# Kernel tuning notes

Hardware: AMD Instinct MI355X
Metric: run time of the kernel (lower is better)

The kernel has to match this reference:

```python
import jax, jax.numpy as jnp
import numpy as np


def _ln(x):
    m = jnp.mean(x, axis=-1, keepdims=True)
    v = jnp.var(x, axis=-1, keepdims=True)
    return (x - m) * jax.lax.rsqrt(v + 1e-5)


def _forward(ql, cl, plm, ada_g_w, ada_g_b, ada_b_w, wq, bq, wk, wv, z_ln_g, z_ln_b, wz, wg, wo, sg_w, sg_b, ada2_g_w, ada2_g_b, ada2_b_w, ff1, ff2, ff3, sg2_w, sg2_b, n_queries, n_keys):
    B, N, C = ql.shape
    NB, _, D = wq.shape
    H = wz.shape[-1]
    DH = D // H
    # AF3-style 32x128 blocked local attention bias (additive mask), as in source
    centers = jnp.arange(N // n_queries + 1, dtype=jnp.float32) * n_queries + (n_queries / 2 - 0.5)
    pos = jnp.arange(N, dtype=jnp.float32)
    row = jnp.abs(pos[:, None] - centers[None, :]) < n_queries / 2   # [N, n_centers]
    col = jnp.abs(pos[:, None] - centers[None, :]) < n_keys / 2     # [N, n_centers]
    BIG = jnp.float32(1e10)
    blm = jnp.sum((row[:, None, :] & col[None, :, :]).astype(jnp.float32), axis=-1) * BIG - BIG  # [N, N], 0 or -1e10
    s_ln = _ln(cl)  # conditioning signal, shared LN across blocks
    a = ql
    for i in range(NB):  # DiffusionTransformer (AF3 Alg 23)
        # AttentionPairBias with AdaLN conditioning (Alg 24/26)
        x = jax.nn.sigmoid(s_ln @ ada_g_w[i] + ada_g_b[i]) * _ln(a) + s_ln @ ada_b_w[i]
        q = (x @ wq[i] + bq[i]).reshape(B, N, H, DH)
        k = (x @ wk[i]).reshape(B, N, H, DH)
        v = (x @ wv[i]).reshape(B, N, H, DH)
        zb = jnp.einsum('bqkc,ch->bhqk', _ln(plm) * z_ln_g[i] + z_ln_b[i], wz[i])  # pair bias
        logits = jnp.einsum('bqhd,bkhd->bhqk', q, k) * (1.0 / np.sqrt(DH)) + zb + blm[None, None]
        p = jax.nn.softmax(logits, axis=-1)
        o = jnp.einsum('bhqk,bkhd->bqhd', p, v)
        g = jax.nn.sigmoid(x @ wg[i]).reshape(B, N, H, DH)
        attn = (g * o).reshape(B, N, D) @ wo[i]
        b_out = jax.nn.sigmoid(s_ln @ sg_w[i] + sg_b[i]) * attn  # adaLN-zero style output gate
        # ConditionedTransitionBlock (Alg 25, SwiGLU)
        y = jax.nn.sigmoid(s_ln @ ada2_g_w[i] + ada2_g_b[i]) * _ln(a) + s_ln @ ada2_b_w[i]
        ff = jax.nn.silu(y @ ff1[i]) * (y @ ff2[i])
        t = jax.nn.sigmoid(s_ln @ sg2_w[i] + sg2_b[i]) * (ff @ ff3[i])
        a = b_out + t
    return a


def setup_inputs() -> dict:
    key = jax.random.key(0)
    B, N, C, CZ = 1, 3072, 128, 16
    H, DH, NB, CT = 4, 32, 3, 256  # CT = n_transition * C
    D = H * DH
    ks = jax.random.split(key, 32)
    it = iter(range(32))
    def r(shape, s=0.02):
        return jax.random.normal(ks[next(it)], shape, dtype=jnp.float32) * s
    inp = {
        'ql': jax.random.normal(ks[next(it)], (B, N, C), jnp.float32),
        'cl': jax.random.normal(ks[next(it)], (B, N, C), jnp.float32),
        'plm': jax.random.normal(ks[next(it)], (B, N, N, CZ), jnp.float32),
        'ada_g_w': r((NB, C, C)), 'ada_g_b': jnp.zeros((NB, C), jnp.float32), 'ada_b_w': r((NB, C, C)),
        'wq': r((NB, C, D)), 'bq': jnp.zeros((NB, D), jnp.float32), 'wk': r((NB, C, D)), 'wv': r((NB, C, D)),
        'z_ln_g': jnp.ones((NB, CZ), jnp.float32), 'z_ln_b': jnp.zeros((NB, CZ), jnp.float32), 'wz': r((NB, CZ, H)),
        'wg': r((NB, C, D)), 'wo': r((NB, D, C)),
        'sg_w': r((NB, C, C)), 'sg_b': jnp.full((NB, C), -2.0, jnp.float32),
        'ada2_g_w': r((NB, C, C)), 'ada2_g_b': jnp.zeros((NB, C), jnp.float32), 'ada2_b_w': r((NB, C, C)),
        'ff1': r((NB, C, CT)), 'ff2': r((NB, C, CT)), 'ff3': r((NB, CT, C)),
        'sg2_w': r((NB, C, C)), 'sg2_b': jnp.full((NB, C), -2.0, jnp.float32),
        'n_queries': 32, 'n_keys': 128,
    }
    return inp


def reference(ql, cl, plm, ada_g_w, ada_g_b, ada_b_w, wq, bq, wk, wv, z_ln_g, z_ln_b, wz, wg, wo, sg_w, sg_b, ada2_g_w, ada2_g_b, ada2_b_w, ff1, ff2, ff3, sg2_w, sg2_b, n_queries, n_keys):
    return _forward(ql, cl, plm, ada_g_w, ada_g_b, ada_b_w, wq, bq, wk, wv, z_ln_g, z_ln_b, wz, wg, wo, sg_w, sg_b, ada2_g_w, ada2_g_b, ada2_b_w, ff1, ff2, ff3, sg2_w, sg2_b, n_queries, n_keys)
```

## Files before the change

### kernel.cpp

```cpp
#include <hip/hip_runtime.h>
#include <cmath>

#define NTOK 3072
#define NBLK 3
#define PSS 133

__device__ __forceinline__ float sig(float v) { return 1.0f / (1.0f + expf(-v)); }

struct Params {
    const float *ql, *cl, *plm;
    const float *ada_g_w, *ada_g_b, *ada_b_w;
    const float *wq, *bq, *wk, *wv;
    const float *z_ln_g, *z_ln_b, *wz;
    const float *wg, *wo, *sg_w, *sg_b;
    const float *ada2_g_w, *ada2_g_b, *ada2_b_w;
    const float *ff1, *ff2, *ff3, *sg2_w, *sg2_b;
    float *anew, *attn, *qkvg, *ffb, *zb, *G;
    float *out;
};

__device__ __forceinline__ float4 ln_row32(float4 v)
{
    float s = v.x + v.y + v.z + v.w;
#pragma unroll
    for (int m = 1; m < 32; m <<= 1) s += __shfl_xor(s, m);
    float mean = s * (1.0f / 128.0f);
    float d0 = v.x - mean, d1 = v.y - mean, d2 = v.z - mean, d3 = v.w - mean;
    float var = d0 * d0 + d1 * d1 + d2 * d2 + d3 * d3;
#pragma unroll
    for (int m = 1; m < 32; m <<= 1) var += __shfl_xor(var, m);
    float rs = 1.0f / sqrtf(var * (1.0f / 128.0f) + 1e-5f);
    return make_float4(d0 * rs, d1 * rs, d2 * rs, d3 * rs);
}

__global__ __launch_bounds__(256) void k0_cond(Params P)
{
    int tid = threadIdx.x, bid = blockIdx.x;
    const size_t NC = (size_t)NTOK * 128;
    if (bid < 1728) {
        __shared__ __align__(16) float smA[32 * 132];
        int x8 = bid & 7, rest = bid >> 3;
        int tl = rest % 12, unit = rest / 12;
        int kind = unit % 6, i = unit / 6;
        int row0 = (x8 * 12 + tl) * 32;
#pragma unroll
        for (int it = 0; it < 4; it++) {
            int fo = (tid + it * 256) * 4, r = fo >> 7, c = fo & 127;
            *(float4*)&smA[r * 132 + c] = *(const float4*)&P.cl[(size_t)(row0 + r) * 128 + c];
        }
        __syncthreads();
        int hw = tid >> 5, cq = (tid & 31) * 4;
#pragma unroll
        for (int rr = 0; rr < 4; rr++) {
            int r = hw * 4 + rr;
            float4 n = ln_row32(*(float4*)&smA[r * 132 + cq]);
            *(float4*)&smA[r * 132 + cq] = n;
        }
        __syncthreads();
        const float* W; const float* bias = nullptr; bool dosig = false;
        switch (kind) {
            case 0:  W = P.ada_g_w  + (size_t)i * 16384; bias = P.ada_g_b  + i * 128; dosig = true; break;
            case 1:  W = P.ada_b_w  + (size_t)i * 16384; break;
            case 2:  W = P.ada2_g_w + (size_t)i * 16384; bias = P.ada2_g_b + i * 128; dosig = true; break;
            case 3:  W = P.ada2_b_w + (size_t)i * 16384; break;
            case 4:  W = P.sg_w     + (size_t)i * 16384; bias = P.sg_b     + i * 128; dosig = true; break;
            default: W = P.sg2_w    + (size_t)i * 16384; bias = P.sg2_b    + i * 128; dosig = true; break;
        }
        W += cq;
        float acc[4][4] = {};
#pragma unroll 8
        for (int k = 0; k < 128; k++) {
            float4 w4 = *(const float4*)(W + (size_t)k * 128);
#pragma unroll
            for (int rr = 0; rr < 4; rr++) {
                float a = smA[(hw * 4 + rr) * 132 + k];
                acc[rr][0] = fmaf(a, w4.x, acc[rr][0]);
                acc[rr][1] = fmaf(a, w4.y, acc[rr][1]);
                acc[rr][2] = fmaf(a, w4.z, acc[rr][2]);
                acc[rr][3] = fmaf(a, w4.w, acc[rr][3]);
            }
        }
        float4 b4 = bias ? *(const float4*)&bias[cq] : make_float4(0, 0, 0, 0);
        float* dst = P.G + (size_t)(kind * NBLK + i) * NC;
#pragma unroll
        for (int rr = 0; rr < 4; rr++) {
            float4 o = make_float4(acc[rr][0] + b4.x, acc[rr][1] + b4.y,
                                   acc[rr][2] + b4.z, acc[rr][3] + b4.w);
            if (dosig) { o.x = sig(o.x); o.y = sig(o.y); o.z = sig(o.z); o.w = sig(o.w); }
            *(float4*)&dst[(size_t)(row0 + hw * 4 + rr) * 128 + cq] = o;
        }
    } else {
        __shared__ __align__(16) float wzg[204];
        int b2 = bid - 1728;
        int x8 = b2 & 7, rest = b2 >> 3;
        int jl = rest >> 2, kkc = rest & 3;
        int j = x8 * 12 + jl;
        if (tid < 192) {
            int i3 = tid >> 6, rem = tid & 63, c = rem >> 2, h = rem & 3;
            wzg[(i3 * 16 + c) * 4 + h] = P.z_ln_g[i3 * 16 + c] * P.wz[(i3 * 16 + c) * 4 + h];
        }
        if (tid < 12) {
            int i3 = tid >> 2, h = tid & 3;
            float s = 0.0f;
            for (int c = 0; c < 16; c++) s += P.z_ln_b[i3 * 16 + c] * P.wz[(i3 * 16 + c) * 4 + h];
            wzg[192 + tid] = s;
        }
        __syncthreads();
        int kstart = max(0, j * 32 - 48);
        int W = min(NTOK, j * 32 + 80) - kstart;
#pragma unroll
        for (int it = 0; it < 4; it++) {
            int idx = tid + it * 256;
            int qi = idx >> 5, kk = kkc * 32 + (idx & 31);
            if (kk >= W) continue;
            int q = j * 32 + qi;
            const float* src = P.plm + ((size_t)q * NTOK + (size_t)(kstart + kk)) * 16;
            float xv[16];
            *(float4*)(xv + 0)  = *(const float4*)(src + 0);
            *(float4*)(xv + 4)  = *(const float4*)(src + 4);
            *(float4*)(xv + 8)  = *(const float4*)(src + 8);
            *(float4*)(xv + 12) = *(const float4*)(src + 12);
            float s = 0.0f;
#pragma unroll
            for (int c = 0; c < 16; c++) s += xv[c];
            float mean = s * (1.0f / 16.0f);
            float var = 0.0f;
#pragma unroll
            for (int c = 0; c < 16; c++) { float d = xv[c] - mean; var += d * d; }
            float rs = 1.0f / sqrtf(var * (1.0f / 16.0f) + 1e-5f);
#pragma unroll
            for (int c = 0; c < 16; c++) xv[c] = (xv[c] - mean) * rs;
#pragma unroll
            for (int i3 = 0; i3 < NBLK; i3++) {
#pragma unroll
                for (int h = 0; h < 4; h++) {
                    float o = wzg[192 + i3 * 4 + h];
#pragma unroll
                    for (int c = 0; c < 16; c++) o = fmaf(xv[c], wzg[(i3 * 16 + c) * 4 + h], o);
                    P.zb[((size_t)(i3 * 4 + h) * NTOK + q) * 128 + kk] = o;
                }
            }
        }
    }
}

__global__ __launch_bounds__(256) void k1_pre(Params P, int i)
{
    __shared__ __align__(16) float smX[32 * 132];
    const size_t NC = (size_t)NTOK * 128;
    int tid = threadIdx.x, bid = blockIdx.x;
    int x8 = bid & 7, rest = bid >> 3;
    int tl = rest % 12, u = rest / 12;
    int row0 = (x8 * 12 + tl) * 32;
    int hw = tid >> 5, cq = (tid & 31) * 4;
    const float* aprev = (i == 0) ? P.ql : P.anew;
    const float* Gg = P.G + (size_t)(((u < 4 ? 0 : 2) * NBLK) + i) * NC;
    const float* Gb = P.G + (size_t)(((u < 4 ? 1 : 3) * NBLK) + i) * NC;
#pragma unroll
    for (int rr = 0; rr < 4; rr++) {
        int r = row0 + hw * 4 + rr;
        float4 a4 = *(const float4*)&aprev[(size_t)r * 128 + cq];
        float4 ln4 = ln_row32(a4);
        float4 g4 = *(const float4*)&Gg[(size_t)r * 128 + cq];
        float4 b4 = *(const float4*)&Gb[(size_t)r * 128 + cq];
        float4 x4;
        x4.x = fmaf(g4.x, ln4.x, b4.x);
        x4.y = fmaf(g4.y, ln4.y, b4.y);
        x4.z = fmaf(g4.z, ln4.z, b4.z);
        x4.w = fmaf(g4.w, ln4.w, b4.w);
        *(float4*)&smX[(hw * 4 + rr) * 132 + cq] = x4;
    }
    __syncthreads();
    if (u < 4) {
        const float* W = (u == 0 ? P.wq : u == 1 ? P.wk : u == 2 ? P.wv : P.wg)
                         + (size_t)i * 16384 + cq;
        float acc[4][4] = {};
#pragma unroll 8
        for (int k = 0; k < 128; k++) {
            float4 w4 = *(const float4*)(W + (size_t)k * 128);
#pragma unroll
            for (int rr = 0; rr < 4; rr++) {
                float a = smX[(hw * 4 + rr) * 132 + k];
                acc[rr][0] = fmaf(a, w4.x, acc[rr][0]);
                acc[rr][1] = fmaf(a, w4.y, acc[rr][1]);
                acc[rr][2] = fmaf(a, w4.z, acc[rr][2]);
                acc[rr][3] = fmaf(a, w4.w, acc[rr][3]);
            }
        }
        float4 b4 = (u == 0) ? *(const float4*)&P.bq[(size_t)i * 128 + cq]
                             : make_float4(0, 0, 0, 0);
#pragma unroll
        for (int rr = 0; rr < 4; rr++) {
            int r = row0 + hw * 4 + rr;
            *(float4*)&P.qkvg[(size_t)r * 512 + u * 128 + cq] =
                make_float4(acc[rr][0] + b4.x, acc[rr][1] + b4.y,
                            acc[rr][2] + b4.z, acc[rr][3] + b4.w);
        }
    } else {
        int ch = (u - 4) * 128;
        const float* W1 = P.ff1 + (size_t)i * 32768 + ch + cq;
        const float* W2 = P.ff2 + (size_t)i * 32768 + ch + cq;
        float a1[4][4] = {}, a2[4][4] = {};
#pragma unroll 4
        for (int k = 0; k < 128; k++) {
            float4 w14 = *(const float4*)(W1 + (size_t)k * 256);
            float4 w24 = *(const float4*)(W2 + (size_t)k * 256);
#pragma unroll
            for (int rr = 0; rr < 4; rr++) {
                float a = smX[(hw * 4 + rr) * 132 + k];
                a1[rr][0] = fmaf(a, w14.x, a1[rr][0]);
                a1[rr][1] = fmaf(a, w14.y, a1[rr][1]);
                a1[rr][2] = fmaf(a, w14.z, a1[rr][2]);
                a1[rr][3] = fmaf(a, w14.w, a1[rr][3]);
                a2[rr][0] = fmaf(a, w24.x, a2[rr][0]);
                a2[rr][1] = fmaf(a, w24.y, a2[rr][1]);
                a2[rr][2] = fmaf(a, w24.z, a2[rr][2]);
                a2[rr][3] = fmaf(a, w24.w, a2[rr][3]);
            }
        }
#pragma unroll
        for (int rr = 0; rr < 4; rr++) {
            int r = row0 + hw * 4 + rr;
            float4 o;
            o.x = a1[rr][0] * sig(a1[rr][0]) * a2[rr][0];
            o.y = a1[rr][1] * sig(a1[rr][1]) * a2[rr][1];
            o.z = a1[rr][2] * sig(a1[rr][2]) * a2[rr][2];
            o.w = a1[rr][3] * sig(a1[rr][3]) * a2[rr][3];
            *(float4*)&P.ffb[(size_t)r * 256 + ch + cq] = o;
        }
    }
}

__global__ __launch_bounds__(256) void k2_attn(Params P, int i)
{
    __shared__ __align__(16) float ks[128 * 36];
    __shared__ __align__(16) float vs[128 * 36];
    __shared__ float ps[32 * PSS];
    int tid = threadIdx.x, bid = blockIdx.x;
    int x8 = bid & 7, g = bid >> 3;
    int h = g / 12, jl = g % 12;
    int j = x8 * 12 + jl;
    int q0 = j * 32;
    int kstart = max(0, q0 - 48);
    int W = min(NTOK, q0 + 80) - kstart;
    for (int idx = tid; idx < W * 8; idx += 256) {
        int kk = idx >> 3, d = (idx & 7) * 4;
        const float* base = &P.qkvg[(size_t)(kstart + kk) * 512 + 128 + h * 32 + d];
        float4 tK = *(const float4*)base;
        float4 tV = *(const float4*)(base + 128);
        *(float4*)&ks[kk * 36 + d] = tK;
        *(float4*)&vs[kk * 36 + d] = tV;
    }
    const float* zbase = &P.zb[((size_t)(i * 4 + h) * NTOK + q0) * 128];
#pragma unroll
    for (int it = 0; it < 4; it++) {
        int idx = tid + it * 256;
        int r = idx >> 5, c4 = (idx & 31) * 4;
        float4 z4 = *(const float4*)&zbase[(size_t)r * 128 + c4];
        ps[r * PSS + c4]     = z4.x;
        ps[r * PSS + c4 + 1] = z4.y;
        ps[r * PSS + c4 + 2] = z4.z;
        ps[r * PSS + c4 + 3] = z4.w;
    }
    int qi = tid & 31, kg = tid >> 5;
    float qreg[32];
    {
        const float* qp = &P.qkvg[(size_t)(q0 + qi) * 512 + h * 32];
#pragma unroll
        for (int d4 = 0; d4 < 8; d4++) {
            float4 tq = *(const float4*)(qp + d4 * 4);
            qreg[d4 * 4] = tq.x; qreg[d4 * 4 + 1] = tq.y;
            qreg[d4 * 4 + 2] = tq.z; qreg[d4 * 4 + 3] = tq.w;
        }
    }
    __syncthreads();
    const float scale = 0.17677669529663687f;
#pragma unroll
    for (int t2 = 0; t2 < 16; t2++) {
        int kk = kg + t2 * 8;
        if (kk < W) {
            float acc = 0.0f;
#pragma unroll
            for (int d4 = 0; d4 < 8; d4++) {
                float4 kv = *(const float4*)&ks[kk * 36 + d4 * 4];
                acc = fmaf(qreg[d4 * 4 + 0], kv.x, acc);
                acc = fmaf(qreg[d4 * 4 + 1], kv.y, acc);
                acc = fmaf(qreg[d4 * 4 + 2], kv.z, acc);
                acc = fmaf(qreg[d4 * 4 + 3], kv.w, acc);
            }
            ps[qi * PSS + kk] = fmaf(acc, scale, ps[qi * PSS + kk]);
        }
    }
    __syncthreads();
    {
        int row = tid >> 3, sub = tid & 7;
        float m = -3.0e38f;
        for (int kk = sub; kk < W; kk += 8) m = fmaxf(m, ps[row * PSS + kk]);
#pragma unroll
        for (int s2 = 1; s2 < 8; s2 <<= 1) m = fmaxf(m, __shfl_xor(m, s2));
        float ssum = 0.0f;
        for (int kk = sub; kk < W; kk += 8) {
            float e = expf(ps[row * PSS + kk] - m);
            ps[row * PSS + kk] = e; ssum += e;
        }
#pragma unroll
        for (int s2 = 1; s2 < 8; s2 <<= 1) ssum += __shfl_xor(ssum, s2);
        float rinv = 1.0f / ssum;
        for (int kk = sub; kk < W; kk += 8) ps[row * PSS + kk] *= rinv;
    }
    __syncthreads();
    {
        int dg = tid >> 5, d0 = dg * 4;
        float o0 = 0, o1 = 0, o2 = 0, o3 = 0;
#pragma unroll 2
        for (int kk = 0; kk < W; kk++) {
            float pv = ps[qi * PSS + kk];
            float4 v4 = *(const float4*)&vs[kk * 36 + d0];
            o0 = fmaf(pv, v4.x, o0);
            o1 = fmaf(pv, v4.y, o1);
            o2 = fmaf(pv, v4.z, o2);
            o3 = fmaf(pv, v4.w, o3);
        }
        float4 g4 = *(const float4*)&P.qkvg[(size_t)(q0 + qi) * 512 + 384 + h * 32 + d0];
        float4 r;
        r.x = o0 * sig(g4.x); r.y = o1 * sig(g4.y);
        r.z = o2 * sig(g4.z); r.w = o3 * sig(g4.w);
        *(float4*)&P.attn[(size_t)(q0 + qi) * 128 + h * 32 + d0] = r;
    }
}

__global__ __launch_bounds__(256) void k3_post(Params P, int i)
{
    __shared__ __align__(16) float smB[16 * 132];
    __shared__ __align__(16) float smC[16 * 260];
    const size_t NC = (size_t)NTOK * 128;
    int tid = threadIdx.x, bid = blockIdx.x;
    int x8 = bid & 7, rest = bid >> 3;
    int tl = rest >> 2, cc = rest & 3;
    int row0 = x8 * 384 + tl * 16;
    int cbase = cc * 32;
#pragma unroll
    for (int it = 0; it < 2; it++) {
        int fo = (tid + it * 256) * 4, r = fo >> 7, c = fo & 127;
        *(float4*)&smB[r * 132 + c] = *(const float4*)&P.attn[(size_t)(row0 + r) * 128 + c];
    }
#pragma unroll
    for (int it = 0; it < 4; it++) {
        int fo = (tid + it * 256) * 4, r = fo >> 8, c = fo & 255;
        *(float4*)&smC[r * 260 + c] = *(const float4*)&P.ffb[(size_t)(row0 + r) * 256 + c];
    }
    __syncthreads();
    int r = tid >> 4, cl2 = (tid & 15) * 2;
    int c = cbase + cl2;
    const float* wo_p = P.wo  + (size_t)i * 16384 + c;
    const float* f3_p = P.ff3 + (size_t)i * 32768 + c;
    float aO0 = 0, aO1 = 0, aT0 = 0, aT1 = 0;
#pragma unroll 8
    for (int k = 0; k < 128; k++) {
        float2 w2 = *(const float2*)(wo_p + (size_t)k * 128);
        float a = smB[r * 132 + k];
        aO0 = fmaf(a, w2.x, aO0);
        aO1 = fmaf(a, w2.y, aO1);
    }
#pragma unroll 8
    for (int k = 0; k < 256; k++) {
        float2 w2 = *(const float2*)(f3_p + (size_t)k * 128);
        float a = smC[r * 260 + k];
        aT0 = fmaf(a, w2.x, aT0);
        aT1 = fmaf(a, w2.y, aT1);
    }
    int row = row0 + r;
    float2 sgv  = *(const float2*)&P.G[(size_t)(4 * NBLK + i) * NC + (size_t)row * 128 + c];
    float2 sg2v = *(const float2*)&P.G[(size_t)(5 * NBLK + i) * NC + (size_t)row * 128 + c];
    float2 o;
    o.x = sgv.x * aO0 + sg2v.x * aT0;
    o.y = sgv.y * aO1 + sg2v.y * aT1;
    float* dst = (i == NBLK - 1) ? P.out : P.anew;
    *(float2*)&dst[(size_t)row * 128 + c] = o;
}

extern "C" void kernel_launch(void* const* d_in, const int* in_sizes, int n_in,
                              void* d_out, int out_size, void* d_ws, size_t ws_size,
                              hipStream_t stream)
{
    Params P;
    P.ql       = (const float*)d_in[0];
    P.cl       = (const float*)d_in[1];
    P.plm      = (const float*)d_in[2];
    P.ada_g_w  = (const float*)d_in[3];
    P.ada_g_b  = (const float*)d_in[4];
    P.ada_b_w  = (const float*)d_in[5];
    P.wq       = (const float*)d_in[6];
    P.bq       = (const float*)d_in[7];
    P.wk       = (const float*)d_in[8];
    P.wv       = (const float*)d_in[9];
    P.z_ln_g   = (const float*)d_in[10];
    P.z_ln_b   = (const float*)d_in[11];
    P.wz       = (const float*)d_in[12];
    P.wg       = (const float*)d_in[13];
    P.wo       = (const float*)d_in[14];
    P.sg_w     = (const float*)d_in[15];
    P.sg_b     = (const float*)d_in[16];
    P.ada2_g_w = (const float*)d_in[17];
    P.ada2_g_b = (const float*)d_in[18];
    P.ada2_b_w = (const float*)d_in[19];
    P.ff1      = (const float*)d_in[20];
    P.ff2      = (const float*)d_in[21];
    P.ff3      = (const float*)d_in[22];
    P.sg2_w    = (const float*)d_in[23];
    P.sg2_b    = (const float*)d_in[24];

    float* ws = (float*)d_ws;
    const size_t NC = (size_t)NTOK * 128;
    P.anew = ws;
    P.attn = ws + NC;
    P.qkvg = ws + 2 * NC;
    P.ffb  = ws + 6 * NC;
    P.zb   = ws + 8 * NC;
    P.G    = ws + 20 * NC;
    P.out  = (float*)d_out;

    k0_cond<<<2112, 256, 0, stream>>>(P);
    for (int i = 0; i < NBLK; i++) {
        k1_pre<<<576, 256, 0, stream>>>(P, i);
        k2_attn<<<384, 256, 0, stream>>>(P, i);
        k3_post<<<768, 256, 0, stream>>>(P, i);
    }
}
```

Baseline: 306.6 us.

## Co-schedule FF3 projection with attention blocks and read K/V directly from global

The attention kernel gains 768 extra blocks that compute the gated FF3 transition output into a new tpart buffer, so that matmul runs concurrently with attention instead of in the post kernel. The post kernel now only does the Wo projection and adds tpart. Attention blocks also drop their K/V shared-memory staging and read K and V straight from global memory, shrinking LDS use and allowing more resident blocks. The cost is repeated uncoalesced global K/V reads across query threads and an extra workspace buffer round trip.

```diff
diff --git a/kernel.cpp b/kernel.cpp
--- a/kernel.cpp
+++ b/kernel.cpp
@@ -15,7 +15,7 @@
     const float *wg, *wo, *sg_w, *sg_b;
     const float *ada2_g_w, *ada2_g_b, *ada2_b_w;
     const float *ff1, *ff2, *ff3, *sg2_w, *sg2_b;
-    float *anew, *attn, *qkvg, *ffb, *zb, *G;
+    float *anew, *attn, *qkvg, *ffb, *zb, *G, *tpart;
     float *out;
 };
 
@@ -233,106 +233,128 @@
 
 __global__ __launch_bounds__(256) void k2_attn(Params P, int i)
 {
-    __shared__ __align__(16) float ks[128 * 36];
-    __shared__ __align__(16) float vs[128 * 36];
-    __shared__ float ps[32 * PSS];
+    __shared__ __align__(16) float ps[32 * PSS];
+    const size_t NC = (size_t)NTOK * 128;
     int tid = threadIdx.x, bid = blockIdx.x;
-    int x8 = bid & 7, g = bid >> 3;
-    int h = g / 12, jl = g % 12;
-    int j = x8 * 12 + jl;
-    int q0 = j * 32;
-    int kstart = max(0, q0 - 48);
-    int W = min(NTOK, q0 + 80) - kstart;
-    for (int idx = tid; idx < W * 8; idx += 256) {
-        int kk = idx >> 3, d = (idx & 7) * 4;
-        const float* base = &P.qkvg[(size_t)(kstart + kk) * 512 + 128 + h * 32 + d];
-        float4 tK = *(const float4*)base;
-        float4 tV = *(const float4*)(base + 128);
-        *(float4*)&ks[kk * 36 + d] = tK;
-        *(float4*)&vs[kk * 36 + d] = tV;
-    }
-    const float* zbase = &P.zb[((size_t)(i * 4 + h) * NTOK + q0) * 128];
-#pragma unroll
-    for (int it = 0; it < 4; it++) {
-        int idx = tid + it * 256;
-        int r = idx >> 5, c4 = (idx & 31) * 4;
-        float4 z4 = *(const float4*)&zbase[(size_t)r * 128 + c4];
-        ps[r * PSS + c4]     = z4.x;
-        ps[r * PSS + c4 + 1] = z4.y;
-        ps[r * PSS + c4 + 2] = z4.z;
-        ps[r * PSS + c4 + 3] = z4.w;
-    }
-    int qi = tid & 31, kg = tid >> 5;
-    float qreg[32];
-    {
-        const float* qp = &P.qkvg[(size_t)(q0 + qi) * 512 + h * 32];
-#pragma unroll
-        for (int d4 = 0; d4 < 8; d4++) {
-            float4 tq = *(const float4*)(qp + d4 * 4);
-            qreg[d4 * 4] = tq.x; qreg[d4 * 4 + 1] = tq.y;
-            qreg[d4 * 4 + 2] = tq.z; qreg[d4 * 4 + 3] = tq.w;
-        }
-    }
-    __syncthreads();
-    const float scale = 0.17677669529663687f;
-#pragma unroll
-    for (int t2 = 0; t2 < 16; t2++) {
-        int kk = kg + t2 * 8;
-        if (kk < W) {
-            float acc = 0.0f;
+    if (bid < 384) {
+        int x8 = bid & 7, g = bid >> 3;
+        int h = g / 12, jl = g % 12;
+        int j = x8 * 12 + jl;
+        int q0 = j * 32;
+        int kstart = max(0, q0 - 48);
+        int W = min(NTOK, q0 + 80) - kstart;
+        const float* zbase = &P.zb[((size_t)(i * 4 + h) * NTOK + q0) * 128];
+#pragma unroll
+        for (int it = 0; it < 4; it++) {
+            int idx = tid + it * 256;
+            int r = idx >> 5, c4 = (idx & 31) * 4;
+            float4 z4 = *(const float4*)&zbase[(size_t)r * 128 + c4];
+            ps[r * PSS + c4]     = z4.x;
+            ps[r * PSS + c4 + 1] = z4.y;
+            ps[r * PSS + c4 + 2] = z4.z;
+            ps[r * PSS + c4 + 3] = z4.w;
+        }
+        int qi = tid & 31, kg = tid >> 5;
+        float qreg[32];
+        {
+            const float* qp = &P.qkvg[(size_t)(q0 + qi) * 512 + h * 32];
 #pragma unroll
             for (int d4 = 0; d4 < 8; d4++) {
-                float4 kv = *(const float4*)&ks[kk * 36 + d4 * 4];
-                acc = fmaf(qreg[d4 * 4 + 0], kv.x, acc);
-                acc = fmaf(qreg[d4 * 4 + 1], kv.y, acc);
-                acc = fmaf(qreg[d4 * 4 + 2], kv.z, acc);
-                acc = fmaf(qreg[d4 * 4 + 3], kv.w, acc);
-            }
-            ps[qi * PSS + kk] = fmaf(acc, scale, ps[qi * PSS + kk]);
-        }
-    }
-    __syncthreads();
-    {
-        int row = tid >> 3, sub = tid & 7;
-        float m = -3.0e38f;
-        for (int kk = sub; kk < W; kk += 8) m = fmaxf(m, ps[row * PSS + kk]);
-#pragma unroll
-        for (int s2 = 1; s2 < 8; s2 <<= 1) m = fmaxf(m, __shfl_xor(m, s2));
-        float ssum = 0.0f;
-        for (int kk = sub; kk < W; kk += 8) {
-            float e = expf(ps[row * PSS + kk] - m);
-            ps[row * PSS + kk] = e; ssum += e;
-        }
-#pragma unroll
-        for (int s2 = 1; s2 < 8; s2 <<= 1) ssum += __shfl_xor(ssum, s2);
-        float rinv = 1.0f / ssum;
-        for (int kk = sub; kk < W; kk += 8) ps[row * PSS + kk] *= rinv;
-    }
-    __syncthreads();
-    {
-        int dg = tid >> 5, d0 = dg * 4;
-        float o0 = 0, o1 = 0, o2 = 0, o3 = 0;
+                float4 tq = *(const float4*)(qp + d4 * 4);
+                qreg[d4 * 4] = tq.x; qreg[d4 * 4 + 1] = tq.y;
+                qreg[d4 * 4 + 2] = tq.z; qreg[d4 * 4 + 3] = tq.w;
+            }
+        }
+        __syncthreads();
+        const float scale = 0.17677669529663687f;
+#pragma unroll
+        for (int t2 = 0; t2 < 16; t2++) {
+            int kk = kg + t2 * 8;
+            if (kk < W) {
+                const float* kp = &P.qkvg[(size_t)(kstart + kk) * 512 + 128 + h * 32];
+                float acc = 0.0f;
+#pragma unroll
+                for (int d4 = 0; d4 < 8; d4++) {
+                    float4 kv = *(const float4*)(kp + d4 * 4);
+                    acc = fmaf(qreg[d4 * 4 + 0], kv.x, acc);
+                    acc = fmaf(qreg[d4 * 4 + 1], kv.y, acc);
+                    acc = fmaf(qreg[d4 * 4 + 2], kv.z, acc);
+                    acc = fmaf(qreg[d4 * 4 + 3], kv.w, acc);
+                }
+                ps[qi * PSS + kk] = fmaf(acc, scale, ps[qi * PSS + kk]);
+            }
+        }
+        __syncthreads();
+        {
+            int row = tid >> 3, sub = tid & 7;
+            float m = -3.0e38f;
+            for (int kk = sub; kk < W; kk += 8) m = fmaxf(m, ps[row * PSS + kk]);
+#pragma unroll
+            for (int s2 = 1; s2 < 8; s2 <<= 1) m = fmaxf(m, __shfl_xor(m, s2));
+            float ssum = 0.0f;
+            for (int kk = sub; kk < W; kk += 8) {
+                float e = expf(ps[row * PSS + kk] - m);
+                ps[row * PSS + kk] = e; ssum += e;
+            }
+#pragma unroll
+            for (int s2 = 1; s2 < 8; s2 <<= 1) ssum += __shfl_xor(ssum, s2);
+            float rinv = 1.0f / ssum;
+            for (int kk = sub; kk < W; kk += 8) ps[row * PSS + kk] *= rinv;
+        }
+        __syncthreads();
+        {
+            int dg = tid >> 5, d0 = dg * 4;
+            const float* vbase = &P.qkvg[(size_t)kstart * 512 + 256 + h * 32 + d0];
+            float o0 = 0, o1 = 0, o2 = 0, o3 = 0;
 #pragma unroll 2
-        for (int kk = 0; kk < W; kk++) {
-            float pv = ps[qi * PSS + kk];
-            float4 v4 = *(const float4*)&vs[kk * 36 + d0];
-            o0 = fmaf(pv, v4.x, o0);
-            o1 = fmaf(pv, v4.y, o1);
-            o2 = fmaf(pv, v4.z, o2);
-            o3 = fmaf(pv, v4.w, o3);
-        }
-        float4 g4 = *(const float4*)&P.qkvg[(size_t)(q0 + qi) * 512 + 384 + h * 32 + d0];
-        float4 r;
-        r.x = o0 * sig(g4.x); r.y = o1 * sig(g4.y);
-        r.z = o2 * sig(g4.z); r.w = o3 * sig(g4.w);
-        *(float4*)&P.attn[(size_t)(q0 + qi) * 128 + h * 32 + d0] = r;
+            for (int kk = 0; kk < W; kk++) {
+                float pv = ps[qi * PSS + kk];
+                float4 v4 = *(const float4*)(vbase + (size_t)kk * 512);
+                o0 = fmaf(pv, v4.x, o0);
+                o1 = fmaf(pv, v4.y, o1);
+                o2 = fmaf(pv, v4.z, o2);
+                o3 = fmaf(pv, v4.w, o3);
+            }
+            float4 g4 = *(const float4*)&P.qkvg[(size_t)(q0 + qi) * 512 + 384 + h * 32 + d0];
+            float4 r;
+            r.x = o0 * sig(g4.x); r.y = o1 * sig(g4.y);
+            r.z = o2 * sig(g4.z); r.w = o3 * sig(g4.w);
+            *(float4*)&P.attn[(size_t)(q0 + qi) * 128 + h * 32 + d0] = r;
+        }
+    } else {
+        float* smC = ps;
+        int b2 = bid - 384;
+        int x8 = b2 & 7, rest = b2 >> 3;
+        int tl = rest >> 2, cc = rest & 3;
+        int row0 = x8 * 384 + tl * 16;
+        int cbase = cc * 32;
+#pragma unroll
+        for (int it = 0; it < 4; it++) {
+            int fo = (tid + it * 256) * 4, r = fo >> 8, c = fo & 255;
+            *(float4*)&smC[r * 260 + c] = *(const float4*)&P.ffb[(size_t)(row0 + r) * 256 + c];
+        }
+        __syncthreads();
+        int r = tid >> 4, cl2 = (tid & 15) * 2;
+        int c = cbase + cl2;
+        const float* f3_p = P.ff3 + (size_t)i * 32768 + c;
+        float aT0 = 0, aT1 = 0;
+#pragma unroll 8
+        for (int k = 0; k < 256; k++) {
+            float2 w2 = *(const float2*)(f3_p + (size_t)k * 128);
+            float a = smC[r * 260 + k];
+            aT0 = fmaf(a, w2.x, aT0);
+            aT1 = fmaf(a, w2.y, aT1);
+        }
+        int row = row0 + r;
+        float2 sg2v = *(const float2*)&P.G[(size_t)(5 * NBLK + i) * NC + (size_t)row * 128 + c];
+        *(float2*)&P.tpart[(size_t)row * 128 + c] =
+            make_float2(sg2v.x * aT0, sg2v.y * aT1);
     }
 }
 
 __global__ __launch_bounds__(256) void k3_post(Params P, int i)
 {
     __shared__ __align__(16) float smB[16 * 132];
-    __shared__ __align__(16) float smC[16 * 260];
     const size_t NC = (size_t)NTOK * 128;
     int tid = threadIdx.x, bid = blockIdx.x;
     int x8 = bid & 7, rest = bid >> 3;
@@ -344,17 +366,11 @@
         int fo = (tid + it * 256) * 4, r = fo >> 7, c = fo & 127;
         *(float4*)&smB[r * 132 + c] = *(const float4*)&P.attn[(size_t)(row0 + r) * 128 + c];
     }
-#pragma unroll
-    for (int it = 0; it < 4; it++) {
-        int fo = (tid + it * 256) * 4, r = fo >> 8, c = fo & 255;
-        *(float4*)&smC[r * 260 + c] = *(const float4*)&P.ffb[(size_t)(row0 + r) * 256 + c];
-    }
     __syncthreads();
     int r = tid >> 4, cl2 = (tid & 15) * 2;
     int c = cbase + cl2;
-    const float* wo_p = P.wo  + (size_t)i * 16384 + c;
-    const float* f3_p = P.ff3 + (size_t)i * 32768 + c;
-    float aO0 = 0, aO1 = 0, aT0 = 0, aT1 = 0;
+    const float* wo_p = P.wo + (size_t)i * 16384 + c;
+    float aO0 = 0, aO1 = 0;
 #pragma unroll 8
     for (int k = 0; k < 128; k++) {
         float2 w2 = *(const float2*)(wo_p + (size_t)k * 128);
@@ -362,19 +378,12 @@
         aO0 = fmaf(a, w2.x, aO0);
         aO1 = fmaf(a, w2.y, aO1);
     }
-#pragma unroll 8
-    for (int k = 0; k < 256; k++) {
-        float2 w2 = *(const float2*)(f3_p + (size_t)k * 128);
-        float a = smC[r * 260 + k];
-        aT0 = fmaf(a, w2.x, aT0);
-        aT1 = fmaf(a, w2.y, aT1);
-    }
     int row = row0 + r;
-    float2 sgv  = *(const float2*)&P.G[(size_t)(4 * NBLK + i) * NC + (size_t)row * 128 + c];
-    float2 sg2v = *(const float2*)&P.G[(size_t)(5 * NBLK + i) * NC + (size_t)row * 128 + c];
+    float2 sgv = *(const float2*)&P.G[(size_t)(4 * NBLK + i) * NC + (size_t)row * 128 + c];
+    float2 tp  = *(const float2*)&P.tpart[(size_t)row * 128 + c];
     float2 o;
-    o.x = sgv.x * aO0 + sg2v.x * aT0;
-    o.y = sgv.y * aO1 + sg2v.y * aT1;
+    o.x = sgv.x * aO0 + tp.x;
+    o.y = sgv.y * aO1 + tp.y;
     float* dst = (i == NBLK - 1) ? P.out : P.anew;
     *(float2*)&dst[(size_t)row * 128 + c] = o;
 }
@@ -412,18 +421,19 @@
 
     float* ws = (float*)d_ws;
     const size_t NC = (size_t)NTOK * 128;
-    P.anew = ws;
-    P.attn = ws + NC;
-    P.qkvg = ws + 2 * NC;
-    P.ffb  = ws + 6 * NC;
-    P.zb   = ws + 8 * NC;
-    P.G    = ws + 20 * NC;
-    P.out  = (float*)d_out;
+    P.anew  = ws;
+    P.attn  = ws + NC;
+    P.qkvg  = ws + 2 * NC;
+    P.ffb   = ws + 6 * NC;
+    P.zb    = ws + 8 * NC;
+    P.G     = ws + 20 * NC;
+    P.tpart = ws + 38 * NC;
+    P.out   = (float*)d_out;
 
     k0_cond<<<2112, 256, 0, stream>>>(P);
     for (int i = 0; i < NBLK; i++) {
         k1_pre<<<576, 256, 0, stream>>>(P, i);
-        k2_attn<<<384, 256, 0, stream>>>(P, i);
+        k2_attn<<<1152, 256, 0, stream>>>(P, i);
         k3_post<<<768, 256, 0, stream>>>(P, i);
     }
 }
```

New measurement: 327.6 us. 6.9% more time.
